# Kernel optimization log

Hardware: AMD Instinct MI355X
Metric: run time of the kernel (lower is better)

Reference implementation:

```python
import jax, jax.numpy as jnp
import numpy as np

B, C, H, W = 16, 256, 32, 32
NH, DH = 16, 16          # n_heads, n_head_channels; NH*DH == C
STRIDE, KK = 2, 9        # offset conv stride / kernel (stage_idx=0)
Hk, Wk = 16, 16          # offset map size = H/stride
NS = Hk * Wk             # n_sample
EPS_LN, EPS_BN = 1e-5, 1e-5


def conv1x1(x, w, b=None):
    # x: [B,Ci,H,W], w: [Co,Ci]
    y = jnp.einsum('bihw,oi->bohw', x, w)
    if b is not None:
        y = y + b[None, :, None, None]
    return y


def dwconv(x, w, b):
    # depthwise conv, w: [C,1,KK,KK]
    y = jax.lax.conv_general_dilated(
        x, w, (STRIDE, STRIDE), [(KK // 2, KK // 2)] * 2,
        dimension_numbers=('NCHW', 'OIHW', 'NCHW'),
        feature_group_count=x.shape[1])
    return y + b[None, :, None, None]


def ln_channels(x, g, b):
    # LayerNormProxy: layer-norm over channel dim of NCHW
    m = jnp.mean(x, axis=1, keepdims=True)
    v = jnp.mean((x - m) ** 2, axis=1, keepdims=True)
    return (x - m) / jnp.sqrt(v + EPS_LN) * g[None, :, None, None] + b[None, :, None, None]


def ref_points(hk, wk, b):
    # normalized (y, x) reference grid in [-1, 1], matching _get_ref_points
    ry = (jnp.arange(hk, dtype=jnp.float32) + 0.5) / hk * 2.0 - 1.0
    rx = (jnp.arange(wk, dtype=jnp.float32) + 0.5) / wk * 2.0 - 1.0
    ref = jnp.stack(jnp.meshgrid(ry, rx, indexing='ij'), axis=-1)  # [hk,wk,2] (y,x)
    return jnp.broadcast_to(ref[None], (b, hk, wk, 2))


def grid_sample_bilinear(img, grid):
    # img: [B,C,H,W]; grid: [B,Hg,Wg,2] in (x,y) order, [-1,1], align_corners=True,
    # zeros padding (matches torch F.grid_sample defaults).
    Bi, Ci, Hi, Wi = img.shape
    gx = (grid[..., 0] + 1.0) * 0.5 * (Wi - 1)
    gy = (grid[..., 1] + 1.0) * 0.5 * (Hi - 1)
    x0 = jnp.floor(gx); y0 = jnp.floor(gy)
    x1 = x0 + 1.0;      y1 = y0 + 1.0
    wx1 = gx - x0; wx0 = 1.0 - wx1
    wy1 = gy - y0; wy0 = 1.0 - wy1
    imgf = img.reshape(Bi, Ci, Hi * Wi)

    def gather(yi, xi):
        valid = (yi >= 0) & (yi < Hi) & (xi >= 0) & (xi < Wi)
        idx = (jnp.clip(yi, 0, Hi - 1) * Wi + jnp.clip(xi, 0, Wi - 1)).astype(jnp.int32)
        v = jnp.take_along_axis(imgf, idx.reshape(Bi, 1, -1), axis=2)  # [B,C,Hg*Wg]
        return v * valid.reshape(Bi, 1, -1).astype(img.dtype)

    out = (gather(y0, x0) * (wy0 * wx0).reshape(Bi, 1, -1)
           + gather(y0, x1) * (wy0 * wx1).reshape(Bi, 1, -1)
           + gather(y1, x0) * (wy1 * wx0).reshape(Bi, 1, -1)
           + gather(y1, x1) * (wy1 * wx1).reshape(Bi, 1, -1))
    return out.reshape(Bi, Ci, grid.shape[1], grid.shape[2])


def setup_inputs() -> dict:
    key = jax.random.key(0)
    ks = jax.random.split(key, 16)
    s = 0.05
    return {
        'x':        jax.random.normal(ks[0], (B, C, H, W), jnp.float32),
        'wq':       jax.random.normal(ks[1], (C, C), jnp.float32) * s,
        'bq':       jax.random.normal(ks[2], (C,), jnp.float32) * s,
        'off_dw_w': jax.random.normal(ks[3], (C, 1, KK, KK), jnp.float32) * s,
        'off_dw_b': jax.random.normal(ks[4], (C,), jnp.float32) * s,
        'ln_g':     jnp.ones((C,), jnp.float32),
        'ln_b':     jnp.zeros((C,), jnp.float32),
        'off_pw_w': jax.random.normal(ks[5], (2, C), jnp.float32) * s,
        'wk':       jax.random.normal(ks[6], (C, C), jnp.float32) * s,
        'bk':       jax.random.normal(ks[7], (C,), jnp.float32) * s,
        'wv':       jax.random.normal(ks[8], (C, C), jnp.float32) * s,
        'bv':       jax.random.normal(ks[9], (C,), jnp.float32) * s,
        'wo':       jax.random.normal(ks[10], (C, C), jnp.float32) * s,
        'bo':       jax.random.normal(ks[11], (C,), jnp.float32) * s,
        'bn_g':     jnp.ones((C,), jnp.float32),
        'bn_b':     jnp.zeros((C,), jnp.float32),
        'bn_m':     jax.random.normal(ks[12], (C,), jnp.float32) * s,
        'bn_v':     jax.random.uniform(ks[13], (C,), jnp.float32) + 0.5,
    }


def reference(x, wq, bq, off_dw_w, off_dw_b, ln_g, ln_b, off_pw_w,
              wk, bk, wv, bv, wo, bo, bn_g, bn_b, bn_m, bn_v):
    q = conv1x1(x, wq, bq)                                 # [B,C,H,W]
    # offset branch (n_groups=1 so q_off == q)
    off = dwconv(q, off_dw_w, off_dw_b)                    # [B,C,Hk,Wk]
    off = jax.nn.gelu(ln_channels(off, ln_g, ln_b), approximate=False)
    offset = jnp.einsum('bihw,oi->bohw', off, off_pw_w)    # [B,2,Hk,Wk] (y,x)
    offset = jnp.transpose(offset, (0, 2, 3, 1))           # [B,Hk,Wk,2]
    ref = ref_points(Hk, Wk, B)
    pos = jnp.tanh(offset + ref)                           # offset_range_factor[0] < 0 branch
    # deformable sampling: grid takes (x,y)
    xs = grid_sample_bilinear(x, pos[..., ::-1])           # [B,C,Hk,Wk]
    xs = xs.reshape(B, C, 1, NS)
    k = conv1x1(xs, wk, bk).reshape(B * NH, DH, NS)
    v = conv1x1(xs, wv, bv).reshape(B * NH, DH, NS)
    qf = q.reshape(B * NH, DH, H * W)
    attn = jnp.einsum('bcm,bcn->bmn', qf, k) * (DH ** -0.5)  # [B*NH, H*W, NS]
    attn = jax.nn.softmax(attn, axis=2)
    out = jnp.einsum('bmn,bcn->bcm', attn, v).reshape(B, C, H, W)
    y = conv1x1(out, wo, bo)
    # BatchNorm2d in eval mode with running stats
    y = ((y - bn_m[None, :, None, None]) / jnp.sqrt(bn_v[None, :, None, None] + EPS_BN)
         * bn_g[None, :, None, None] + bn_b[None, :, None, None])
    return y
```

## Files before the change

### kernel.cpp

```cpp
#include <hip/hip_runtime.h>
#include <hip/hip_bf16.h>
#include <math.h>

#define BATCH 16
#define CH    256
#define HW    1024
#define NS    256
#define NH    16
#define DH    16

typedef __attribute__((ext_vector_type(8))) short short8v;
typedef __attribute__((ext_vector_type(4))) float float4v;

__device__ __forceinline__ unsigned short f2bf(float f) {
    return __builtin_bit_cast(unsigned short, __float2bfloat16(f));
}
__device__ __forceinline__ unsigned pack2(float lo, float hi) {
    return (unsigned)f2bf(lo) | ((unsigned)f2bf(hi) << 16);
}

__global__ __launch_bounds__(256) void prep_k(
    const float* __restrict__ wq, const float* __restrict__ wk,
    const float* __restrict__ wv, const float* __restrict__ wo,
    unsigned short* __restrict__ Wf,
    const float* __restrict__ x, unsigned short* __restrict__ xT)
{
    int blk = blockIdx.x;
    if (blk < 1024) {
        const float* W;
        switch (blk >> 8) {
            case 0: W = wq; break;
            case 1: W = wk; break;
            case 2: W = wv; break;
            default: W = wo; break;
        }
        int e = (blk & 255) * 256 + threadIdx.x;
        int i = e & 7, l = (e >> 3) & 63, kt = (e >> 9) & 7, ot = e >> 12;
        float v = W[(ot * 16 + (l & 15)) * 256 + kt * 32 + 8 * (l >> 4) + i];
        Wf[(blk >> 8) * 65536 + e] = f2bf(v);
    } else {
        int xb = blk - 1024;
        int b = xb >> 4, pblk = (xb >> 2) & 3, cblk = xb & 3;
        int p = pblk * 256 + threadIdx.x;
        const float* xp = x + (size_t)b * CH * HW + p;
        unsigned short* o = xT + ((size_t)b * HW + p) * CH;
        #pragma unroll
        for (int cc = 0; cc < 64; cc += 8) {
            int c0 = cblk * 64 + cc;
            short8v t;
            #pragma unroll
            for (int i = 0; i < 8; ++i) t[i] = (short)f2bf(xp[(size_t)(c0 + i) * HW]);
            *(short8v*)&o[c0] = t;
        }
    }
}

template<int P, int MODE>
__global__ __launch_bounds__(256) void gemm_k(
    const unsigned short* __restrict__ Wf, const unsigned short* __restrict__ XT,
    const float* __restrict__ bias, const float* __restrict__ bias2,
    float* __restrict__ outF, unsigned short* __restrict__ outB,
    unsigned short* __restrict__ outB2,
    const float* __restrict__ bn_g, const float* __restrict__ bn_b,
    const float* __restrict__ bn_m, const float* __restrict__ bn_v)
{
    const int bz  = blockIdx.z;
    const int b   = (MODE == 1) ? (bz & 15) : bz;
    const int mat = (MODE == 1) ? (bz >> 4) : 0;
    const unsigned short* Wfm = Wf + mat * 65536;

    const int t = threadIdx.x, lane = t & 63, wvi = t >> 6;
    const int g = lane >> 4, col = lane & 15;
    const int o0 = blockIdx.x * 64;
    const int p0 = blockIdx.y * 128 + wvi * 32;
    const unsigned short* xb = XT + ((size_t)b * P + p0) * CH;

    float4v acc[4][2];
    #pragma unroll
    for (int mi = 0; mi < 4; ++mi)
        #pragma unroll
        for (int ni = 0; ni < 2; ++ni) {
            float4v z = {0.f, 0.f, 0.f, 0.f};
            acc[mi][ni] = z;
        }

    #pragma unroll
    for (int kt = 0; kt < 8; ++kt) {
        short8v af[4], bf[2];
        #pragma unroll
        for (int mi = 0; mi < 4; ++mi)
            af[mi] = *(const short8v*)&Wfm[(((((o0 >> 4) + mi) * 8) + kt) * 64 + lane) * 8];
        #pragma unroll
        for (int ni = 0; ni < 2; ++ni)
            bf[ni] = *(const short8v*)&xb[(size_t)(ni * 16 + col) * CH + kt * 32 + 8 * g];
        #pragma unroll
        for (int mi = 0; mi < 4; ++mi)
            #pragma unroll
            for (int ni = 0; ni < 2; ++ni)
                acc[mi][ni] = __builtin_amdgcn_mfma_f32_16x16x32_bf16(
                    af[mi], bf[ni], acc[mi][ni], 0, 0, 0);
    }

    const float* bp = (MODE == 1 && mat == 1) ? bias2 : bias;
    #pragma unroll
    for (int mi = 0; mi < 4; ++mi) {
        const int ob = o0 + mi * 16 + 4 * g;
        float bs[4];
        #pragma unroll
        for (int ii = 0; ii < 4; ++ii) bs[ii] = bp[ob + ii];

        if (MODE == 2) {
            float sc[4], sh[4];
            #pragma unroll
            for (int ii = 0; ii < 4; ++ii) {
                int o = ob + ii;
                float s = bn_g[o] * rsqrtf(bn_v[o] + 1e-5f);
                sc[ii] = s;
                sh[ii] = bn_b[o] - bn_m[o] * s + bs[ii] * s;
            }
            #pragma unroll
            for (int ni = 0; ni < 2; ++ni) {
                int p = p0 + ni * 16 + col;
                #pragma unroll
                for (int ii = 0; ii < 4; ++ii)
                    outF[((size_t)(b * CH + ob + ii)) * P + p] =
                        acc[mi][ni][ii] * sc[ii] + sh[ii];
            }
        } else {
            #pragma unroll
            for (int ni = 0; ni < 2; ++ni) {
                int p = p0 + ni * 16 + col;
                float v0 = acc[mi][ni][0] + bs[0];
                float v1 = acc[mi][ni][1] + bs[1];
                float v2 = acc[mi][ni][2] + bs[2];
                float v3 = acc[mi][ni][3] + bs[3];
                if (MODE == 0) {
                    outF[((size_t)(b * CH + ob + 0)) * P + p] = v0;
                    outF[((size_t)(b * CH + ob + 1)) * P + p] = v1;
                    outF[((size_t)(b * CH + ob + 2)) * P + p] = v2;
                    outF[((size_t)(b * CH + ob + 3)) * P + p] = v3;
                    uint2 w;
                    w.x = pack2(v0 * 0.25f, v1 * 0.25f);
                    w.y = pack2(v2 * 0.25f, v3 * 0.25f);
                    *(uint2*)&outB[((size_t)(b * P + p)) * CH + ob] = w;
                } else {
                    if (mat == 0) {
                        uint2 w;
                        w.x = pack2(v0, v1);
                        w.y = pack2(v2, v3);
                        *(uint2*)&outB[((size_t)(b * P + p)) * CH + ob] = w;
                    } else {
                        outB2[((size_t)(b * CH + ob + 0)) * P + p] = f2bf(v0);
                        outB2[((size_t)(b * CH + ob + 1)) * P + p] = f2bf(v1);
                        outB2[((size_t)(b * CH + ob + 2)) * P + p] = f2bf(v2);
                        outB2[((size_t)(b * CH + ob + 3)) * P + p] = f2bf(v3);
                    }
                }
            }
        }
    }
}

__global__ __launch_bounds__(256) void dwconv_k(
    const float* __restrict__ q, const float* __restrict__ w,
    const float* __restrict__ bias, float* __restrict__ off)
{
    int bc = blockIdx.x;
    int c  = bc & (CH - 1);
    __shared__ float plane[HW];
    __shared__ float kw[81];
    int t = threadIdx.x;
    const float* qp = q + (size_t)bc * HW;
    #pragma unroll
    for (int j = t; j < HW; j += 256) plane[j] = qp[j];
    if (t < 81) kw[t] = w[c * 81 + t];
    __syncthreads();
    int hk = t >> 4, wk = t & 15;
    float s = bias[c];
    int yb = hk * 2 - 4, xb = wk * 2 - 4;
    #pragma unroll
    for (int dy = 0; dy < 9; ++dy) {
        int yy = yb + dy;
        if ((unsigned)yy < 32u) {
            #pragma unroll
            for (int dx = 0; dx < 9; ++dx) {
                int xx = xb + dx;
                if ((unsigned)xx < 32u) s += kw[dy * 9 + dx] * plane[yy * 32 + xx];
            }
        }
    }
    off[(size_t)bc * NS + t] = s;
}

__device__ inline void block_reduce2(float& a, float& b, int t, float* sbuf)
{
    #pragma unroll
    for (int o = 32; o > 0; o >>= 1) {
        a += __shfl_down(a, o);
        b += __shfl_down(b, o);
    }
    int w = t >> 6;
    if ((t & 63) == 0) { sbuf[w * 2] = a; sbuf[w * 2 + 1] = b; }
    __syncthreads();
    a = sbuf[0] + sbuf[2] + sbuf[4] + sbuf[6];
    b = sbuf[1] + sbuf[3] + sbuf[5] + sbuf[7];
    __syncthreads();
}

__global__ __launch_bounds__(256) void lngs_k(
    const float* __restrict__ off, const float* __restrict__ ln_g,
    const float* __restrict__ ln_b, const float* __restrict__ pw,
    const float* __restrict__ x, unsigned short* __restrict__ xsT)
{
    __shared__ float sbuf[8];
    int bs = blockIdx.x;
    int b = bs >> 8, s = bs & 255;
    int c = threadIdx.x;
    float v = off[((size_t)(b * CH + c)) * NS + s];
    float a = v, q2 = v * v;
    block_reduce2(a, q2, c, sbuf);
    float mean = a * (1.0f / 256.0f);
    float var  = q2 * (1.0f / 256.0f) - mean * mean;
    float xn = (v - mean) * rsqrtf(var + 1e-5f) * ln_g[c] + ln_b[c];
    float g = 0.5f * xn * (1.0f + erff(xn * 0.70710678118654752f));
    float d0 = g * pw[c];
    float d1 = g * pw[CH + c];
    block_reduce2(d0, d1, c, sbuf);

    int hk = s >> 4, wk = s & 15;
    float ry = ((hk + 0.5f) / 16.0f) * 2.0f - 1.0f;
    float rx = ((wk + 0.5f) / 16.0f) * 2.0f - 1.0f;
    float py = tanhf(d0 + ry);
    float px = tanhf(d1 + rx);

    float gx = (px + 1.0f) * 0.5f * 31.0f;
    float gy = (py + 1.0f) * 0.5f * 31.0f;
    float x0f = floorf(gx), y0f = floorf(gy);
    int ix = (int)x0f, iy = (int)y0f;
    float wx1 = gx - x0f, wx0 = 1.0f - wx1;
    float wy1 = gy - y0f, wy0 = 1.0f - wy1;
    const float* img = x + ((size_t)b * CH + c) * HW;
    float v00 = ((unsigned)iy < 32u && (unsigned)ix < 32u) ? img[iy * 32 + ix] : 0.0f;
    float v01 = ((unsigned)iy < 32u && (unsigned)(ix + 1) < 32u) ? img[iy * 32 + ix + 1] : 0.0f;
    float v10 = ((unsigned)(iy + 1) < 32u && (unsigned)ix < 32u) ? img[(iy + 1) * 32 + ix] : 0.0f;
    float v11 = ((unsigned)(iy + 1) < 32u && (unsigned)(ix + 1) < 32u) ? img[(iy + 1) * 32 + ix + 1] : 0.0f;
    float vv = wy0 * wx0 * v00 + wy0 * wx1 * v01 + wy1 * wx0 * v10 + wy1 * wx1 * v11;
    xsT[(size_t)bs * CH + c] = f2bf(vv);
}

__global__ __launch_bounds__(256) void attn_mfma_k(
    const unsigned short* __restrict__ qT, const unsigned short* __restrict__ kT,
    const unsigned short* __restrict__ vbf, unsigned short* __restrict__ aoT)
{
    const int bh   = blockIdx.x >> 2;
    const int mseg = blockIdx.x & 3;
    const int b = bh >> 4, h = bh & 15;

    __shared__ short Kp[16 * 32 * 8 + 8];
    __shared__ short Vsh[16 * 256];
    __shared__ short Ps[4][16 * 32];

    const int tid  = threadIdx.x;
    const int lane = tid & 63;
    const int wvi  = tid >> 6;
    const int col  = lane & 15;
    const int g    = lane >> 4;

    for (int e = tid; e < 512; e += 256) {
        int t = e >> 5, l = e & 31, gg = l >> 4, c = l & 15;
        short8v kk = *(const short8v*)&kT[((size_t)(b * NS + 16 * t + c)) * CH + h * 16 + 8 * gg];
        *(short8v*)&Kp[(t * 32 + l) * 8] = kk;
    }
    if (tid == 0) {
        short8v z = {0, 0, 0, 0, 0, 0, 0, 0};
        *(short8v*)&Kp[16 * 32 * 8] = z;
    }
    {
        const unsigned short* Vb = vbf + ((size_t)(b * CH + h * 16)) * NS;
        int d = tid >> 4, n0 = (tid & 15) * 16;
        char* vb = (char*)Vsh;
        #pragma unroll
        for (int hh = 0; hh < 2; ++hh) {
            short8v pk = *(const short8v*)&Vb[(size_t)d * NS + n0 + 8 * hh];
            *(short8v*)(vb + ((d * 512 + (n0 + 8 * hh) * 2) ^ ((d & 7) << 4))) = pk;
        }
    }
    __syncthreads();

    const unsigned short* Qb = qT + (size_t)b * HW * CH + h * 16;
    unsigned short*       Ob = aoT + (size_t)b * HW * CH + h * 16;
    char* pbase = (char*)Ps[wvi];
    const char* kbase = (const char*)Kp + ((lane < 32) ? lane * 16 : 16 * 32 * 16);
    const int   kstep = (lane < 32) ? 512 : 0;

    for (int mt = 0; mt < 4; ++mt) {
        const int m0 = mseg * 256 + wvi * 64 + mt * 16;

        short8v qf = {0, 0, 0, 0, 0, 0, 0, 0};
        if (g < 2)
            qf = *(const short8v*)&Qb[(size_t)(m0 + col) * CH + 8 * g];

        float4v p[16];
        #pragma unroll
        for (int t = 0; t < 16; ++t) {
            short8v kf = *(const short8v*)(kbase + t * kstep);
            float4v z = {0.f, 0.f, 0.f, 0.f};
            p[t] = __builtin_amdgcn_mfma_f32_16x16x32_bf16(kf, qf, z, 0, 0, 0);
        }

        float mx4[16];
        #pragma unroll
        for (int t = 0; t < 16; ++t)
            mx4[t] = fmaxf(fmaxf(p[t][0], p[t][1]), fmaxf(p[t][2], p[t][3]));
        #pragma unroll
        for (int o = 8; o >= 1; o >>= 1)
            #pragma unroll
            for (int i = 0; i < 8; ++i)
                if (i < o) mx4[i] = fmaxf(mx4[i], mx4[i + o]);
        float mx = mx4[0];
        mx = fmaxf(mx, __shfl_xor(mx, 16));
        mx = fmaxf(mx, __shfl_xor(mx, 32));

        float s4[4] = {0.f, 0.f, 0.f, 0.f};
        #pragma unroll
        for (int t = 0; t < 16; ++t) {
            #pragma unroll
            for (int i = 0; i < 4; ++i) {
                float e = __expf(p[t][i] - mx);
                p[t][i] = e;
                s4[i] += e;
            }
        }
        float sum = (s4[0] + s4[1]) + (s4[2] + s4[3]);
        sum += __shfl_xor(sum, 16);
        sum += __shfl_xor(sum, 32);
        const float inv = 1.0f / sum;

        float4v acc = {0.f, 0.f, 0.f, 0.f};
        #pragma unroll
        for (int c = 0; c < 8; ++c) {
            #pragma unroll
            for (int pp = 0; pp < 2; ++pp) {
                float4v pv = p[2 * c + pp];
                uint2 wr;
                wr.x = pack2(pv[0], pv[1]);
                wr.y = pack2(pv[2], pv[3]);
                *(uint2*)(pbase + ((col * 64 + (16 * pp + 4 * g) * 2) ^ ((col & 7) << 4))) = wr;
            }
            short8v pf = *(const short8v*)(pbase + ((col * 64 + 16 * g) ^ ((col & 7) << 4)));
            short8v vf = *(const short8v*)((char*)Vsh + ((col * 512 + 64 * c + 16 * g) ^ ((col & 7) << 4)));
            acc = __builtin_amdgcn_mfma_f32_16x16x32_bf16(vf, pf, acc, 0, 0, 0);
        }

        uint2 w;
        w.x = pack2(acc[0] * inv, acc[1] * inv);
        w.y = pack2(acc[2] * inv, acc[3] * inv);
        *(uint2*)&Ob[(size_t)(m0 + col) * CH + 4 * g] = w;
    }
}

extern "C" void kernel_launch(void* const* d_in, const int* in_sizes, int n_in,
                              void* d_out, int out_size, void* d_ws, size_t ws_size,
                              hipStream_t stream)
{
    const float* x        = (const float*)d_in[0];
    const float* wq       = (const float*)d_in[1];
    const float* bq       = (const float*)d_in[2];
    const float* off_dw_w = (const float*)d_in[3];
    const float* off_dw_b = (const float*)d_in[4];
    const float* ln_g     = (const float*)d_in[5];
    const float* ln_b     = (const float*)d_in[6];
    const float* off_pw_w = (const float*)d_in[7];
    const float* wk       = (const float*)d_in[8];
    const float* bk       = (const float*)d_in[9];
    const float* wv       = (const float*)d_in[10];
    const float* bv       = (const float*)d_in[11];
    const float* wo       = (const float*)d_in[12];
    const float* bo       = (const float*)d_in[13];
    const float* bn_g     = (const float*)d_in[14];
    const float* bn_b     = (const float*)d_in[15];
    const float* bn_m     = (const float*)d_in[16];
    const float* bn_v     = (const float*)d_in[17];

    float* ws  = (float*)d_ws;
    float* q   = ws;
    float* off = q + 4194304;
    unsigned short* us  = (unsigned short*)(off + 1048576);
    unsigned short* Wf  = us;
    unsigned short* xT  = Wf  + 262144;
    unsigned short* qT  = xT  + 4194304;
    unsigned short* xsT = qT  + 4194304;
    unsigned short* kT  = xsT + 1048576;
    unsigned short* vbf = kT  + 1048576;
    unsigned short* aoT = vbf + 1048576;

    prep_k<<<1280, 256, 0, stream>>>(wq, wk, wv, wo, Wf, x, xT);
    gemm_k<HW, 0><<<dim3(4, 8, BATCH), 256, 0, stream>>>(
        Wf, xT, bq, nullptr, q, qT, nullptr, nullptr, nullptr, nullptr, nullptr);
    dwconv_k<<<BATCH * CH, 256, 0, stream>>>(q, off_dw_w, off_dw_b, off);
    lngs_k<<<BATCH * NS, 256, 0, stream>>>(off, ln_g, ln_b, off_pw_w, x, xsT);
    gemm_k<NS, 1><<<dim3(4, 2, 2 * BATCH), 256, 0, stream>>>(
        Wf + 65536, xsT, bk, bv, nullptr, kT, vbf, nullptr, nullptr, nullptr, nullptr);
    attn_mfma_k<<<BATCH * NH * 4, 256, 0, stream>>>(qT, kT, vbf, aoT);
    gemm_k<HW, 2><<<dim3(4, 8, BATCH), 256, 0, stream>>>(
        Wf + 3 * 65536, aoT, bo, nullptr, (float*)d_out, nullptr, nullptr,
        bn_g, bn_b, bn_m, bn_v);
}
```

Measured before the change: 117.6 us.

## Fuse all stages into one persistent cooperative kernel with grid syncs

Replaces the seven separate kernel launches with a single cooperative persistent kernel. Each stage runs as a grid-stride loop over work units, stages are separated by grid.sync(), and the stages share one static shared-memory buffer. The aim is to remove launch gaps and per-kernel tail effects. In exchange, occupancy is tied to the maximum register and shared-memory use across all stages, the grid size is capped at 1024 blocks, and grid-wide barriers add their own cost.

```diff
diff --git a/kernel.cpp b/kernel.cpp
--- a/kernel.cpp
+++ b/kernel.cpp
@@ -1,6 +1,9 @@
 #include <hip/hip_runtime.h>
+#include <hip/hip_cooperative_groups.h>
 #include <hip/hip_bf16.h>
 #include <math.h>
+
+namespace cg = cooperative_groups;
 
 #define BATCH 16
 #define CH    256
@@ -19,13 +22,12 @@
     return (unsigned)f2bf(lo) | ((unsigned)f2bf(hi) << 16);
 }
 
-__global__ __launch_bounds__(256) void prep_k(
-    const float* __restrict__ wq, const float* __restrict__ wk,
+__device__ __forceinline__ void prep_unit(
+    int blk, const float* __restrict__ wq, const float* __restrict__ wk,
     const float* __restrict__ wv, const float* __restrict__ wo,
     unsigned short* __restrict__ Wf,
     const float* __restrict__ x, unsigned short* __restrict__ xT)
 {
-    int blk = blockIdx.x;
     if (blk < 1024) {
         const float* W;
         switch (blk >> 8) {
@@ -56,7 +58,8 @@
 }
 
 template<int P, int MODE>
-__global__ __launch_bounds__(256) void gemm_k(
+__device__ __forceinline__ void gemm_unit(
+    int ox, int py, int bz,
     const unsigned short* __restrict__ Wf, const unsigned short* __restrict__ XT,
     const float* __restrict__ bias, const float* __restrict__ bias2,
     float* __restrict__ outF, unsigned short* __restrict__ outB,
@@ -64,15 +67,14 @@
     const float* __restrict__ bn_g, const float* __restrict__ bn_b,
     const float* __restrict__ bn_m, const float* __restrict__ bn_v)
 {
-    const int bz  = blockIdx.z;
     const int b   = (MODE == 1) ? (bz & 15) : bz;
     const int mat = (MODE == 1) ? (bz >> 4) : 0;
     const unsigned short* Wfm = Wf + mat * 65536;
 
     const int t = threadIdx.x, lane = t & 63, wvi = t >> 6;
     const int g = lane >> 4, col = lane & 15;
-    const int o0 = blockIdx.x * 64;
-    const int p0 = blockIdx.y * 128 + wvi * 32;
+    const int o0 = ox * 64;
+    const int p0 = py * 128 + wvi * 32;
     const unsigned short* xb = XT + ((size_t)b * P + p0) * CH;
 
     float4v acc[4][2];
@@ -89,7 +91,7 @@
         short8v af[4], bf[2];
         #pragma unroll
         for (int mi = 0; mi < 4; ++mi)
-            af[mi] = *(const short8v*)&Wfm[(((((o0 >> 4) + mi) * 8) + kt) * 64 + lane) * 8];
+            af[mi] = *(const short8v*)&Wfm[((((ox * 4 + mi) * 8) + kt) * 64 + lane) * 8];
         #pragma unroll
         for (int ni = 0; ni < 2; ++ni)
             bf[ni] = *(const short8v*)&xb[(size_t)(ni * 16 + col) * CH + kt * 32 + 8 * g];
@@ -161,14 +163,12 @@
     }
 }
 
-__global__ __launch_bounds__(256) void dwconv_k(
+__device__ __forceinline__ void dwconv_unit(
+    int bc, float* plane, float* kw,
     const float* __restrict__ q, const float* __restrict__ w,
     const float* __restrict__ bias, float* __restrict__ off)
 {
-    int bc = blockIdx.x;
-    int c  = bc & (CH - 1);
-    __shared__ float plane[HW];
-    __shared__ float kw[81];
+    int c = bc & (CH - 1);
     int t = threadIdx.x;
     const float* qp = q + (size_t)bc * HW;
     #pragma unroll
@@ -190,9 +190,10 @@
         }
     }
     off[(size_t)bc * NS + t] = s;
-}
-
-__device__ inline void block_reduce2(float& a, float& b, int t, float* sbuf)
+    __syncthreads();
+}
+
+__device__ __forceinline__ void block_reduce2(float& a, float& b, int t, float* sbuf)
 {
     #pragma unroll
     for (int o = 32; o > 0; o >>= 1) {
@@ -207,13 +208,12 @@
     __syncthreads();
 }
 
-__global__ __launch_bounds__(256) void lngs_k(
+__device__ __forceinline__ void lngs_unit(
+    int bs, float* sbuf,
     const float* __restrict__ off, const float* __restrict__ ln_g,
     const float* __restrict__ ln_b, const float* __restrict__ pw,
     const float* __restrict__ x, unsigned short* __restrict__ xsT)
 {
-    __shared__ float sbuf[8];
-    int bs = blockIdx.x;
     int b = bs >> 8, s = bs & 255;
     int c = threadIdx.x;
     float v = off[((size_t)(b * CH + c)) * NS + s];
@@ -248,17 +248,14 @@
     xsT[(size_t)bs * CH + c] = f2bf(vv);
 }
 
-__global__ __launch_bounds__(256) void attn_mfma_k(
+__device__ __forceinline__ void attn_unit(
+    int u, short* Kp, short* Vsh, short* Ps,
     const unsigned short* __restrict__ qT, const unsigned short* __restrict__ kT,
     const unsigned short* __restrict__ vbf, unsigned short* __restrict__ aoT)
 {
-    const int bh   = blockIdx.x >> 2;
-    const int mseg = blockIdx.x & 3;
+    const int bh   = u >> 2;
+    const int mseg = u & 3;
     const int b = bh >> 4, h = bh & 15;
-
-    __shared__ short Kp[16 * 32 * 8 + 8];
-    __shared__ short Vsh[16 * 256];
-    __shared__ short Ps[4][16 * 32];
 
     const int tid  = threadIdx.x;
     const int lane = tid & 63;
@@ -289,7 +286,7 @@
 
     const unsigned short* Qb = qT + (size_t)b * HW * CH + h * 16;
     unsigned short*       Ob = aoT + (size_t)b * HW * CH + h * 16;
-    char* pbase = (char*)Ps[wvi];
+    char* pbase = (char*)(Ps + wvi * 512);
     const char* kbase = (const char*)Kp + ((lane < 32) ? lane * 16 : 16 * 32 * 16);
     const int   kstep = (lane < 32) ? 512 : 0;
 
@@ -357,6 +354,56 @@
         w.y = pack2(acc[2] * inv, acc[3] * inv);
         *(uint2*)&Ob[(size_t)(m0 + col) * CH + 4 * g] = w;
     }
+    __syncthreads();
+}
+
+__global__ __launch_bounds__(256) void fused_k(
+    const float* x, const float* wq, const float* bq,
+    const float* off_dw_w, const float* off_dw_b,
+    const float* ln_g, const float* ln_b, const float* off_pw_w,
+    const float* wk, const float* bk, const float* wv, const float* bv,
+    const float* wo, const float* bo,
+    const float* bn_g, const float* bn_b, const float* bn_m, const float* bn_v,
+    float* q, float* off, unsigned short* Wf, unsigned short* xT,
+    unsigned short* qT, unsigned short* xsT, unsigned short* kT,
+    unsigned short* vbf, unsigned short* aoT, float* out)
+{
+    cg::grid_group grid = cg::this_grid();
+    __shared__ __align__(16) char smem[20496];
+    const int nb = gridDim.x;
+    const int bid = blockIdx.x;
+
+    for (int u = bid; u < 1280; u += nb)
+        prep_unit(u, wq, wk, wv, wo, Wf, x, xT);
+    grid.sync();
+
+    for (int u = bid; u < 512; u += nb)
+        gemm_unit<HW, 0>(u & 3, (u >> 2) & 7, u >> 5, Wf, xT, bq, nullptr,
+                         q, qT, nullptr, nullptr, nullptr, nullptr, nullptr);
+    grid.sync();
+
+    for (int u = bid; u < 4096; u += nb)
+        dwconv_unit(u, (float*)smem, (float*)(smem + 16384),
+                    q, off_dw_w, off_dw_b, off);
+    grid.sync();
+
+    for (int u = bid; u < 4096; u += nb)
+        lngs_unit(u, (float*)smem, off, ln_g, ln_b, off_pw_w, x, xsT);
+    grid.sync();
+
+    for (int u = bid; u < 256; u += nb)
+        gemm_unit<NS, 1>(u & 3, (u >> 2) & 1, u >> 3, Wf + 65536, xsT, bk, bv,
+                         nullptr, kT, vbf, nullptr, nullptr, nullptr, nullptr);
+    grid.sync();
+
+    for (int u = bid; u < 1024; u += nb)
+        attn_unit(u, (short*)smem, (short*)(smem + 8208),
+                  (short*)(smem + 16400), qT, kT, vbf, aoT);
+    grid.sync();
+
+    for (int u = bid; u < 512; u += nb)
+        gemm_unit<HW, 2>(u & 3, (u >> 2) & 7, u >> 5, Wf + 3 * 65536, aoT, bo,
+                         nullptr, out, nullptr, nullptr, bn_g, bn_b, bn_m, bn_v);
 }
 
 extern "C" void kernel_launch(void* const* d_in, const int* in_sizes, int n_in,
@@ -393,16 +440,23 @@
     unsigned short* kT  = xsT + 1048576;
     unsigned short* vbf = kT  + 1048576;
     unsigned short* aoT = vbf + 1048576;
-
-    prep_k<<<1280, 256, 0, stream>>>(wq, wk, wv, wo, Wf, x, xT);
-    gemm_k<HW, 0><<<dim3(4, 8, BATCH), 256, 0, stream>>>(
-        Wf, xT, bq, nullptr, q, qT, nullptr, nullptr, nullptr, nullptr, nullptr);
-    dwconv_k<<<BATCH * CH, 256, 0, stream>>>(q, off_dw_w, off_dw_b, off);
-    lngs_k<<<BATCH * NS, 256, 0, stream>>>(off, ln_g, ln_b, off_pw_w, x, xsT);
-    gemm_k<NS, 1><<<dim3(4, 2, 2 * BATCH), 256, 0, stream>>>(
-        Wf + 65536, xsT, bk, bv, nullptr, kT, vbf, nullptr, nullptr, nullptr, nullptr);
-    attn_mfma_k<<<BATCH * NH * 4, 256, 0, stream>>>(qT, kT, vbf, aoT);
-    gemm_k<HW, 2><<<dim3(4, 8, BATCH), 256, 0, stream>>>(
-        Wf + 3 * 65536, aoT, bo, nullptr, (float*)d_out, nullptr, nullptr,
-        bn_g, bn_b, bn_m, bn_v);
-}
+    float* out = (float*)d_out;
+
+    int maxb = 0;
+    hipOccupancyMaxActiveBlocksPerMultiprocessor(&maxb, fused_k, 256, 0);
+    if (maxb < 1) maxb = 1;
+    long long grid = (long long)maxb * 256;
+    if (grid > 1024) grid = 1024;
+
+    void* kargs[] = {
+        (void*)&x, (void*)&wq, (void*)&bq, (void*)&off_dw_w, (void*)&off_dw_b,
+        (void*)&ln_g, (void*)&ln_b, (void*)&off_pw_w,
+        (void*)&wk, (void*)&bk, (void*)&wv, (void*)&bv,
+        (void*)&wo, (void*)&bo,
+        (void*)&bn_g, (void*)&bn_b, (void*)&bn_m, (void*)&bn_v,
+        (void*)&q, (void*)&off, (void*)&Wf, (void*)&xT,
+        (void*)&qT, (void*)&xsT, (void*)&kT, (void*)&vbf, (void*)&aoT, (void*)&out
+    };
+    hipLaunchCooperativeKernel((const void*)fused_k, dim3((unsigned)grid), dim3(256),
+                               kargs, 0, stream);
+}
```

Measured after the change: 387.9 us. 3.3x slower.

## Store q, k and attention output in head-major layout for contiguous per-head access

Applied to the files above, without the earlier changes.

Changes the bf16 q, k and attention-output buffers from [B, P, C] to a head-major [B, NH, P, 16] layout. The producing GEMMs write per-head blocks and the final GEMM reads per-head blocks, so the attention kernel loads Q and K and stores its output as contiguous 32-byte rows instead of 32-byte pieces at a 512-byte stride. This trades scattered accesses in attention for differently strided reads and writes in the GEMM epilogues and in the output projection's B-operand loads.

```diff
diff --git a/kernel.cpp b/kernel.cpp
--- a/kernel.cpp
+++ b/kernel.cpp
@@ -91,8 +91,15 @@
         for (int mi = 0; mi < 4; ++mi)
             af[mi] = *(const short8v*)&Wfm[(((((o0 >> 4) + mi) * 8) + kt) * 64 + lane) * 8];
         #pragma unroll
-        for (int ni = 0; ni < 2; ++ni)
-            bf[ni] = *(const short8v*)&xb[(size_t)(ni * 16 + col) * CH + kt * 32 + 8 * g];
+        for (int ni = 0; ni < 2; ++ni) {
+            if (MODE == 2) {
+                const int hh = kt * 2 + (g >> 1);
+                const int p  = p0 + ni * 16 + col;
+                bf[ni] = *(const short8v*)&XT[(((size_t)(b * 16 + hh) * P + p) << 4) + 8 * (g & 1)];
+            } else {
+                bf[ni] = *(const short8v*)&xb[(size_t)(ni * 16 + col) * CH + kt * 32 + 8 * g];
+            }
+        }
         #pragma unroll
         for (int mi = 0; mi < 4; ++mi)
             #pragma unroll
@@ -127,6 +134,7 @@
                         acc[mi][ni][ii] * sc[ii] + sh[ii];
             }
         } else {
+            const int hh = (o0 >> 4) + mi;
             #pragma unroll
             for (int ni = 0; ni < 2; ++ni) {
                 int p = p0 + ni * 16 + col;
@@ -142,13 +150,13 @@
                     uint2 w;
                     w.x = pack2(v0 * 0.25f, v1 * 0.25f);
                     w.y = pack2(v2 * 0.25f, v3 * 0.25f);
-                    *(uint2*)&outB[((size_t)(b * P + p)) * CH + ob] = w;
+                    *(uint2*)&outB[(((size_t)(b * 16 + hh) * P + p) << 4) + 4 * g] = w;
                 } else {
                     if (mat == 0) {
                         uint2 w;
                         w.x = pack2(v0, v1);
                         w.y = pack2(v2, v3);
-                        *(uint2*)&outB[((size_t)(b * P + p)) * CH + ob] = w;
+                        *(uint2*)&outB[(((size_t)(b * 16 + hh) * P + p) << 4) + 4 * g] = w;
                     } else {
                         outB2[((size_t)(b * CH + ob + 0)) * P + p] = f2bf(v0);
                         outB2[((size_t)(b * CH + ob + 1)) * P + p] = f2bf(v1);
@@ -249,8 +257,8 @@
 }
 
 __global__ __launch_bounds__(256) void attn_mfma_k(
-    const unsigned short* __restrict__ qT, const unsigned short* __restrict__ kT,
-    const unsigned short* __restrict__ vbf, unsigned short* __restrict__ aoT)
+    const unsigned short* __restrict__ qH, const unsigned short* __restrict__ kH,
+    const unsigned short* __restrict__ vbf, unsigned short* __restrict__ aoH)
 {
     const int bh   = blockIdx.x >> 2;
     const int mseg = blockIdx.x & 3;
@@ -266,9 +274,10 @@
     const int col  = lane & 15;
     const int g    = lane >> 4;
 
+    const unsigned short* kHb = kH + ((size_t)(b * 16 + h) * NS << 4);
     for (int e = tid; e < 512; e += 256) {
         int t = e >> 5, l = e & 31, gg = l >> 4, c = l & 15;
-        short8v kk = *(const short8v*)&kT[((size_t)(b * NS + 16 * t + c)) * CH + h * 16 + 8 * gg];
+        short8v kk = *(const short8v*)&kHb[((16 * t + c) << 4) + 8 * gg];
         *(short8v*)&Kp[(t * 32 + l) * 8] = kk;
     }
     if (tid == 0) {
@@ -287,8 +296,8 @@
     }
     __syncthreads();
 
-    const unsigned short* Qb = qT + (size_t)b * HW * CH + h * 16;
-    unsigned short*       Ob = aoT + (size_t)b * HW * CH + h * 16;
+    const unsigned short* Qb = qH + ((size_t)(b * 16 + h) * HW << 4);
+    unsigned short*       Ob = aoH + ((size_t)(b * 16 + h) * HW << 4);
     char* pbase = (char*)Ps[wvi];
     const char* kbase = (const char*)Kp + ((lane < 32) ? lane * 16 : 16 * 32 * 16);
     const int   kstep = (lane < 32) ? 512 : 0;
@@ -298,7 +307,7 @@
 
         short8v qf = {0, 0, 0, 0, 0, 0, 0, 0};
         if (g < 2)
-            qf = *(const short8v*)&Qb[(size_t)(m0 + col) * CH + 8 * g];
+            qf = *(const short8v*)&Qb[((m0 + col) << 4) + 8 * g];
 
         float4v p[16];
         #pragma unroll
@@ -355,7 +364,7 @@
         uint2 w;
         w.x = pack2(acc[0] * inv, acc[1] * inv);
         w.y = pack2(acc[2] * inv, acc[3] * inv);
-        *(uint2*)&Ob[(size_t)(m0 + col) * CH + 4 * g] = w;
+        *(uint2*)&Ob[((m0 + col) << 4) + 4 * g] = w;
     }
 }
 
@@ -388,21 +397,21 @@
     unsigned short* us  = (unsigned short*)(off + 1048576);
     unsigned short* Wf  = us;
     unsigned short* xT  = Wf  + 262144;
-    unsigned short* qT  = xT  + 4194304;
-    unsigned short* xsT = qT  + 4194304;
-    unsigned short* kT  = xsT + 1048576;
-    unsigned short* vbf = kT  + 1048576;
-    unsigned short* aoT = vbf + 1048576;
+    unsigned short* qH  = xT  + 4194304;
+    unsigned short* xsT = qH  + 4194304;
+    unsigned short* kH  = xsT + 1048576;
+    unsigned short* vbf = kH  + 1048576;
+    unsigned short* aoH = vbf + 1048576;
 
     prep_k<<<1280, 256, 0, stream>>>(wq, wk, wv, wo, Wf, x, xT);
     gemm_k<HW, 0><<<dim3(4, 8, BATCH), 256, 0, stream>>>(
-        Wf, xT, bq, nullptr, q, qT, nullptr, nullptr, nullptr, nullptr, nullptr);
+        Wf, xT, bq, nullptr, q, qH, nullptr, nullptr, nullptr, nullptr, nullptr);
     dwconv_k<<<BATCH * CH, 256, 0, stream>>>(q, off_dw_w, off_dw_b, off);
     lngs_k<<<BATCH * NS, 256, 0, stream>>>(off, ln_g, ln_b, off_pw_w, x, xsT);
     gemm_k<NS, 1><<<dim3(4, 2, 2 * BATCH), 256, 0, stream>>>(
-        Wf + 65536, xsT, bk, bv, nullptr, kT, vbf, nullptr, nullptr, nullptr, nullptr);
-    attn_mfma_k<<<BATCH * NH * 4, 256, 0, stream>>>(qT, kT, vbf, aoT);
+        Wf + 65536, xsT, bk, bv, nullptr, kH, vbf, nullptr, nullptr, nullptr, nullptr);
+    attn_mfma_k<<<BATCH * NH * 4, 256, 0, stream>>>(qH, kH, vbf, aoH);
     gemm_k<HW, 2><<<dim3(4, 8, BATCH), 256, 0, stream>>>(
-        Wf + 3 * 65536, aoT, bo, nullptr, (float*)d_out, nullptr, nullptr,
+        Wf + 3 * 65536, aoH, bo, nullptr, (float*)d_out, nullptr, nullptr,
         bn_g, bn_b, bn_m, bn_v);
 }
```

Measured after the change: 111.7 us. -5.0%, faster.
